# Performance work log

Measured on AMD Instinct MI355X. Metric: run time of the kernel, lower is better.

Reference implementation:

```python
import jax, jax.numpy as jnp
import numpy as np

B, P, K = 32, 1024, 20  # clouds, points per cloud, kNN neighbors
EPS = 1e-5


def knn_idx(x, k):
    # x: [B,P,d] -> indices of k nearest neighbors (squared L2, includes self), [B,P,k]
    d2 = jnp.sum(x * x, axis=-1)
    dist = d2[:, :, None] + d2[:, None, :] - 2.0 * jnp.einsum('bpd,bqd->bpq', x, x)
    _, idx = jax.lax.top_k(-dist, k)
    return idx


def edge_conv(x, idx, msg_fn):
    # gather neighbor features, build [x_i, x_j - x_i] edge features, max-aggregate
    xj = jax.vmap(lambda xb, ib: xb[ib])(x, idx)            # [B,P,K,d]
    xi = jnp.broadcast_to(x[:, :, None, :], xj.shape)       # [B,P,K,d]
    e = jnp.concatenate([xi, xj - xi], axis=-1)             # [B,P,K,2d]
    return jnp.max(msg_fn(e), axis=2)                       # [B,P,out]


def setup_inputs() -> dict:
    key = jax.random.key(0)
    ks = jax.random.split(key, 5)
    s = 0.05
    return {
        'pos': jax.random.normal(ks[0], (B * P, 3), jnp.float32),
        'W1a': jax.random.normal(ks[1], (6, 64), jnp.float32) * s,
        'b1a': jnp.zeros((64,), jnp.float32),
        'g1': jnp.ones((64,), jnp.float32),
        'be1': jnp.zeros((64,), jnp.float32),
        'W1b': jax.random.normal(ks[2], (64, 64), jnp.float32) * s,
        'b1b': jnp.zeros((64,), jnp.float32),
        'W2': jax.random.normal(ks[3], (128, 128), jnp.float32) * s,
        'b2': jnp.zeros((128,), jnp.float32),
        'Wl': jax.random.normal(ks[4], (192, 128), jnp.float32) * s,
        'bl': jnp.zeros((128,), jnp.float32),
        'batch': jnp.repeat(jnp.arange(B, dtype=jnp.int32), P),
    }


def reference(pos, W1a, b1a, g1, be1, W1b, b1b, W2, b2, Wl, bl, batch):
    # batch is uniform-sized and sorted -> fixed reshape to [B,P,.]
    x0 = pos.reshape(B, P, 3)

    def mlp1(e):  # Linear(6,64) -> BatchNorm -> ReLU -> Linear(64,64)
        h = e @ W1a + b1a
        mu = jnp.mean(h, axis=(0, 1, 2))
        var = jnp.var(h, axis=(0, 1, 2))
        h = (h - mu) * jax.lax.rsqrt(var + EPS) * g1 + be1
        h = jax.nn.relu(h)
        return h @ W1b + b1b

    x1 = edge_conv(x0, knn_idx(x0, K), mlp1)                         # [B,P,64]
    x2 = edge_conv(x1, knn_idx(x1, K), lambda e: e @ W2 + b2)        # [B,P,128]
    h = jnp.concatenate([x1, x2], axis=-1) @ Wl + bl                 # [B,P,128]
    return jnp.max(h, axis=1)                                        # global_max_pool -> [B,128]
```

## Files before the change

kernel.cpp:

```cpp
#include <hip/hip_runtime.h>
#include <cfloat>
#include <cstdint>

#define NB 32
#define NP 1024
#define NK 20
#define NPTS 32768

typedef __attribute__((ext_vector_type(8))) short bf16x8;
typedef __attribute__((ext_vector_type(4))) float f32x4;

__device__ __forceinline__ unsigned bf16rne(float v) {
  const unsigned u = __float_as_uint(v);
  return (u + 0x7fffu + ((u >> 16) & 1u)) >> 16;
}

__global__ __launch_bounds__(256) void kd2(const float* __restrict__ x, int dim,
                                           float* __restrict__ d2) {
  int p = blockIdx.x * 256 + threadIdx.x;
  if (p >= NPTS) return;
  if (dim == 64) {
    const float4* xr = (const float4*)(x + (size_t)p * 64);
    float s = 0.f;
#pragma unroll
    for (int dq = 0; dq < 16; dq++) {
      float4 v = xr[dq];
      s = fmaf(v.x, v.x, s);
      s = fmaf(v.y, v.y, s);
      s = fmaf(v.z, v.z, s);
      s = fmaf(v.w, v.w, s);
    }
    d2[p] = s;
  } else {
    float s = 0.f;
#pragma unroll
    for (int d = 0; d < 3; d++) {
      float v = x[p * 3 + d];
      s = fmaf(v, v, s);
    }
    d2[p] = s;
  }
}

__global__ __launch_bounds__(256) void kxprep(const float* __restrict__ x,
                                              unsigned short* __restrict__ Xh,
                                              unsigned short* __restrict__ Xl) {
  const int t = blockIdx.x * 256 + threadIdx.x;
  const int p = t >> 3, g = t & 7;
  const float4* xr = (const float4*)(x + (size_t)p * 64 + g * 8);
  const float4 v0 = xr[0];
  const float4 v1 = xr[1];
  const float vv[8] = {v0.x, v0.y, v0.z, v0.w, v1.x, v1.y, v1.z, v1.w};
  unsigned short h[8], l[8];
#pragma unroll
  for (int j = 0; j < 8; j++) {
    const float z = vv[j];
    const unsigned u = __float_as_uint(z);
    const unsigned hb = (u + 0x7fffu + ((u >> 16) & 1u)) & 0xffff0000u;
    h[j] = (unsigned short)(hb >> 16);
    l[j] = (unsigned short)bf16rne(z - __uint_as_float(hb));
  }
  const int off = (((p >> 4) * 2 + (g >> 2)) * 64 + ((g & 3) << 4) + (p & 15)) * 8;
  *(uint4*)&Xh[off] = *(const uint4*)&h[0];
  *(uint4*)&Xl[off] = *(const uint4*)&l[0];
}

__global__ __launch_bounds__(256) void kdistm(const unsigned short* __restrict__ Xh,
                                              const unsigned short* __restrict__ Xl,
                                              const float* __restrict__ d2,
                                              int c0, int nc, float* __restrict__ D) {
  const int lane = threadIdx.x & 63;
  const int w = threadIdx.x >> 6;
  const int cloud = blockIdx.x % nc;
  const int t = blockIdx.x / nc;
  const int tr0 = (t >> 3) * 128, tc0 = (t & 7) * 128;
  const int cb = (c0 + cloud) * 1024;
  const int rw = tr0 + w * 32;

  bf16x8 Ah[2][2], Al[2][2];
#pragma unroll
  for (int mt = 0; mt < 2; mt++)
#pragma unroll
    for (int ks = 0; ks < 2; ks++) {
      const int tg = (cb + rw + mt * 16) >> 4;
      const size_t base = ((size_t)(tg * 2 + ks) * 64 + lane) * 8;
      Ah[mt][ks] = *(const bf16x8*)&Xh[base];
      Al[mt][ks] = *(const bf16x8*)&Xl[base];
    }
  float d2r[2][4];
#pragma unroll
  for (int mt = 0; mt < 2; mt++)
#pragma unroll
    for (int r = 0; r < 4; r++)
      d2r[mt][r] = d2[cb + rw + mt * 16 + (lane >> 4) * 4 + r];

  for (int nt = 0; nt < 8; nt++) {
    const int cg = cb + tc0 + nt * 16;
    bf16x8 Bh2[2], Bl2[2];
#pragma unroll
    for (int ks = 0; ks < 2; ks++) {
      const int tg = cg >> 4;
      const size_t base = ((size_t)(tg * 2 + ks) * 64 + lane) * 8;
      Bh2[ks] = *(const bf16x8*)&Xh[base];
      Bl2[ks] = *(const bf16x8*)&Xl[base];
    }
    const float d2c = d2[cg + (lane & 15)];
#pragma unroll
    for (int mt = 0; mt < 2; mt++) {
      f32x4 C = {0.f, 0.f, 0.f, 0.f};
      C = __builtin_amdgcn_mfma_f32_16x16x32_bf16(Ah[mt][0], Bh2[0], C, 0, 0, 0);
      C = __builtin_amdgcn_mfma_f32_16x16x32_bf16(Ah[mt][0], Bl2[0], C, 0, 0, 0);
      C = __builtin_amdgcn_mfma_f32_16x16x32_bf16(Al[mt][0], Bh2[0], C, 0, 0, 0);
      C = __builtin_amdgcn_mfma_f32_16x16x32_bf16(Ah[mt][1], Bh2[1], C, 0, 0, 0);
      C = __builtin_amdgcn_mfma_f32_16x16x32_bf16(Ah[mt][1], Bl2[1], C, 0, 0, 0);
      C = __builtin_amdgcn_mfma_f32_16x16x32_bf16(Al[mt][1], Bh2[1], C, 0, 0, 0);
#pragma unroll
      for (int r = 0; r < 4; r++) {
        const int row = cloud * 1024 + rw + mt * 16 + (lane >> 4) * 4 + r;
        const int col = tc0 + nt * 16 + (lane & 15);
        D[(size_t)row * 1024 + col] = fmaf(-2.f, C[r], d2r[mt][r] + d2c);
      }
    }
  }
}

template <int DIM>
__global__ __launch_bounds__(256) void kdist(const float* __restrict__ x,
                                             const float* __restrict__ d2,
                                             int c0, int nc, float* __restrict__ D) {
  constexpr int KC = (DIM == 64) ? 32 : 3;
  __shared__ float As[KC][132];
  __shared__ float Bs[KC][132];
  const int tid = threadIdx.x;
  const int cloud = blockIdx.x % nc;
  const int t = blockIdx.x / nc;
  const int tr0 = (t >> 3) * 128, tc0 = (t & 7) * 128;
  const int cb = (c0 + cloud) * 1024;
  const int tr = tid >> 4, tc = tid & 15;

  float acc[8][8];
#pragma unroll
  for (int i = 0; i < 8; i++)
#pragma unroll
    for (int j = 0; j < 8; j++) acc[i][j] = 0.f;

  for (int kc = 0; kc < DIM; kc += KC) {
    __syncthreads();
    if constexpr (DIM == 64) {
      const int row = tid >> 1, seg = tid & 1;
      const float4* sa = (const float4*)(x + (size_t)(cb + tr0 + row) * 64 + kc + seg * 16);
      const float4* sb = (const float4*)(x + (size_t)(cb + tc0 + row) * 64 + kc + seg * 16);
#pragma unroll
      for (int i = 0; i < 4; i++) {
        float4 va = sa[i];
        float4 vb = sb[i];
        const int k0 = seg * 16 + i * 4;
        As[k0 + 0][row] = va.x;
        As[k0 + 1][row] = va.y;
        As[k0 + 2][row] = va.z;
        As[k0 + 3][row] = va.w;
        Bs[k0 + 0][row] = vb.x;
        Bs[k0 + 1][row] = vb.y;
        Bs[k0 + 2][row] = vb.z;
        Bs[k0 + 3][row] = vb.w;
      }
    } else {
      if (tid < 128) {
#pragma unroll
        for (int d = 0; d < 3; d++) {
          As[d][tid] = x[(size_t)(cb + tr0 + tid) * 3 + d];
          Bs[d][tid] = x[(size_t)(cb + tc0 + tid) * 3 + d];
        }
      }
    }
    __syncthreads();
#pragma unroll
    for (int k = 0; k < KC; k++) {
      float a[8], b[8];
      *(float4*)&a[0] = *(const float4*)&As[k][tr * 8];
      *(float4*)&a[4] = *(const float4*)&As[k][tr * 8 + 4];
      *(float4*)&b[0] = *(const float4*)&Bs[k][tc * 8];
      *(float4*)&b[4] = *(const float4*)&Bs[k][tc * 8 + 4];
#pragma unroll
      for (int i = 0; i < 8; i++)
#pragma unroll
        for (int j = 0; j < 8; j++) acc[i][j] = fmaf(a[i], b[j], acc[i][j]);
    }
  }
  float d2r[8], d2c[8];
#pragma unroll
  for (int i = 0; i < 8; i++) d2r[i] = d2[cb + tr0 + tr * 8 + i];
#pragma unroll
  for (int j = 0; j < 8; j++) d2c[j] = d2[cb + tc0 + tc * 8 + j];
#pragma unroll
  for (int i = 0; i < 8; i++) {
    float o[8];
#pragma unroll
    for (int j = 0; j < 8; j++) o[j] = fmaf(-2.f, acc[i][j], d2r[i] + d2c[j]);
    float* dst = &D[(size_t)(cloud * 1024 + tr0 + tr * 8 + i) * 1024 + tc0 + tc * 8];
    *(float4*)&dst[0] = *(const float4*)&o[0];
    *(float4*)&dst[4] = *(const float4*)&o[4];
  }
}

__global__ __launch_bounds__(256) void kselect(const float* __restrict__ D,
                                               int c0, int* __restrict__ idxo) {
  __shared__ unsigned long long lw[4][64];
  const int lane = threadIdx.x & 63;
  const int sub = threadIdx.x >> 6;
  const int pchunk = blockIdx.x * 4 + sub;
  const int pg = c0 * 1024 + pchunk;
  const int gbase = (pg >> 10) << 10;

  unsigned k32[16];
  const float4* dr = (const float4*)(D + (size_t)pchunk * 1024 + lane * 4);
#pragma unroll
  for (int i = 0; i < 4; i++) {
    const float4 d4 = dr[i * 64];
    const float dv[4] = {d4.x, d4.y, d4.z, d4.w};
#pragma unroll
    for (int j = 0; j < 4; j++) {
      unsigned u = __float_as_uint(dv[j]);
      u ^= (((int)u >> 31) | 0x80000000u);
      k32[i * 4 + j] = u;
    }
  }

  unsigned mn = k32[0], mx = k32[0];
#pragma unroll
  for (int i = 1; i < 16; i++) {
    mn = k32[i] < mn ? k32[i] : mn;
    mx = k32[i] > mx ? k32[i] : mx;
  }
#pragma unroll
  for (int s = 1; s < 64; s <<= 1) {
    const unsigned a = __shfl_xor(mn, s, 64);
    const unsigned b = __shfl_xor(mx, s, 64);
    mn = a < mn ? a : mn;
    mx = b > mx ? b : mx;
  }

  unsigned long long midk = 0;
  bool found = false;
  {
    unsigned long long lo = mn, hi = (unsigned long long)mx + 1;
    for (int it = 0; it < 33 && !found; ++it) {
      if (hi - lo <= 1) break;
      const unsigned long long m2 = lo + ((hi - lo) >> 1);
      const unsigned m32 = (unsigned)m2;
      int cnt = 0;
#pragma unroll
      for (int i = 0; i < 16; i++) cnt += (k32[i] < m32) ? 1 : 0;
#pragma unroll
      for (int s = 1; s < 64; s <<= 1) cnt += __shfl_xor(cnt, s, 64);
      if (cnt < 20)
        lo = m2;
      else if (cnt > 63)
        hi = m2;
      else {
        midk = (m2 << 10);
        found = true;
      }
    }
  }
  if (!found) {
    unsigned long long key[16];
#pragma unroll
    for (int i = 0; i < 4; i++)
#pragma unroll
      for (int j = 0; j < 4; j++)
        key[i * 4 + j] = ((unsigned long long)k32[i * 4 + j] << 10) |
                         (unsigned)(i * 256 + lane * 4 + j);
    unsigned long long mn64 = key[0], mx64 = key[0];
#pragma unroll
    for (int i = 1; i < 16; i++) {
      mn64 = key[i] < mn64 ? key[i] : mn64;
      mx64 = key[i] > mx64 ? key[i] : mx64;
    }
#pragma unroll
    for (int s = 1; s < 64; s <<= 1) {
      const unsigned long long a = __shfl_xor(mn64, s, 64);
      const unsigned long long b = __shfl_xor(mx64, s, 64);
      mn64 = a < mn64 ? a : mn64;
      mx64 = b > mx64 ? b : mx64;
    }
    unsigned long long lo = mn64, hi = mx64 + 1;
    bool f2 = false;
    for (int it = 0; it < 48 && !f2; ++it) {
      const unsigned long long m2 = lo + ((hi - lo) >> 1);
      int cnt = 0;
#pragma unroll
      for (int i = 0; i < 16; i++) cnt += (key[i] < m2) ? 1 : 0;
#pragma unroll
      for (int s = 1; s < 64; s <<= 1) cnt += __shfl_xor(cnt, s, 64);
      if (cnt < 20)
        lo = m2;
      else if (cnt > 63)
        hi = m2;
      else {
        midk = m2;
        f2 = true;
      }
    }
  }

  unsigned mask = 0;
  unsigned long long key64[16];
#pragma unroll
  for (int i = 0; i < 4; i++)
#pragma unroll
    for (int j = 0; j < 4; j++) {
      const int ii = i * 4 + j;
      key64[ii] = ((unsigned long long)k32[ii] << 10) |
                  (unsigned)(i * 256 + lane * 4 + j);
      mask |= (key64[ii] < midk) ? (1u << ii) : 0u;
    }
  const int lc = __popc(mask);
  int x = lc;
#pragma unroll
  for (int s = 1; s < 64; s <<= 1) {
    const int y = __shfl_up(x, s, 64);
    if (lane >= s) x += y;
  }
  int off = x - lc;
  unsigned long long* w = lw[sub];
  w[lane] = ~0ULL;
  __builtin_amdgcn_wave_barrier();
#pragma unroll
  for (int i = 0; i < 16; i++) {
    if ((mask & (1u << i)) && off < 64) {
      w[off] = key64[i];
      off++;
    }
  }
  __builtin_amdgcn_wave_barrier();
  const unsigned long long K = w[lane];
  int rank = 0;
#pragma unroll
  for (int m = 0; m < 64; m++) rank += (K > w[m]) ? 1 : 0;
  if (K != ~0ULL && rank < NK)
    idxo[(size_t)pg * NK + rank] = gbase + (int)(K & 1023u);
}

__global__ __launch_bounds__(256) void kstats(const float* __restrict__ pos,
                                              const int* __restrict__ idx,
                                              double* __restrict__ Spart) {
  __shared__ float red[4][42];
  const int tid = threadIdx.x;
  const int w = tid >> 6;
  int p = blockIdx.x * 256 + tid;
  float xi0 = pos[p * 3], xi1 = pos[p * 3 + 1], xi2 = pos[p * 3 + 2];
  float s1[6];
  float s2[36];
#pragma unroll
  for (int a = 0; a < 6; a++) s1[a] = 0.f;
#pragma unroll
  for (int a = 0; a < 36; a++) s2[a] = 0.f;
  for (int k = 0; k < NK; k++) {
    int j = idx[p * NK + k];
    float e[6];
    e[0] = xi0;
    e[1] = xi1;
    e[2] = xi2;
    e[3] = pos[j * 3] - xi0;
    e[4] = pos[j * 3 + 1] - xi1;
    e[5] = pos[j * 3 + 2] - xi2;
#pragma unroll
    for (int a = 0; a < 6; a++) {
      s1[a] += e[a];
#pragma unroll
      for (int b = 0; b < 6; b++) s2[a * 6 + b] = fmaf(e[a], e[b], s2[a * 6 + b]);
    }
  }
#pragma unroll
  for (int a = 0; a < 6; a++) {
#pragma unroll
    for (int m = 1; m < 64; m <<= 1) s1[a] += __shfl_xor(s1[a], m, 64);
  }
#pragma unroll
  for (int a = 0; a < 36; a++) {
#pragma unroll
    for (int m = 1; m < 64; m <<= 1) s2[a] += __shfl_xor(s2[a], m, 64);
  }
  if ((tid & 63) == 0) {
#pragma unroll
    for (int a = 0; a < 6; a++) red[w][a] = s1[a];
#pragma unroll
    for (int a = 0; a < 36; a++) red[w][6 + a] = s2[a];
  }
  __syncthreads();
  if (tid < 42) {
    double t = (double)red[0][tid] + (double)red[1][tid] + (double)red[2][tid] +
               (double)red[3][tid];
    Spart[(size_t)blockIdx.x * 42 + tid] = t;
  }
}

__global__ void kbn(const double* __restrict__ Spart, const float* __restrict__ W1a,
                    const float* __restrict__ b1a, const float* __restrict__ g1,
                    const float* __restrict__ be1, const float* __restrict__ W1b,
                    float* __restrict__ ss, unsigned short* __restrict__ Bh,
                    unsigned short* __restrict__ Bl) {
  __shared__ double S[42];
  const int c = threadIdx.x;
  if (c < 42) {
    double t = 0.0;
    for (int b = 0; b < 128; b++) t += Spart[(size_t)b * 42 + c];
    S[c] = t;
  }
  for (int t = c; t < 4096; t += 256) {
    const int j = t & 7, L = (t >> 3) & 63, f = t >> 9;
    const int nt = f >> 1, ks = f & 1;
    const int k = ks * 32 + (L >> 4) * 8 + j;
    const int n = nt * 16 + (L & 15);
    const float wv = W1b[k * 64 + n];
    const unsigned u = __float_as_uint(wv);
    const unsigned hb = (u + 0x7fffu + ((u >> 16) & 1u)) & 0xffff0000u;
    Bh[t] = (unsigned short)(hb >> 16);
    Bl[t] = (unsigned short)bf16rne(wv - __uint_as_float(hb));
  }
  __syncthreads();
  if (c < 64) {
    double w[6];
#pragma unroll
    for (int d = 0; d < 6; d++) w[d] = (double)W1a[d * 64 + c];
    double b = (double)b1a[c];
    const double invN = 1.0 / (double)((size_t)NPTS * NK);
    double m1 = 0.0;
#pragma unroll
    for (int d = 0; d < 6; d++) m1 += w[d] * S[d];
    m1 *= invN;
    double q = 0.0;
#pragma unroll
    for (int a = 0; a < 6; a++)
#pragma unroll
      for (int d = 0; d < 6; d++) q += w[a] * w[d] * S[6 + a * 6 + d];
    q *= invN;
    double mu = m1 + b;
    double eh2 = q + 2.0 * b * m1 + b * b;
    double var = eh2 - mu * mu;
    if (var < 0.0) var = 0.0;
    double inv = 1.0 / sqrt(var + 1e-5);
    double sc = (double)g1[c] * inv;
    ss[c] = (float)sc;
    ss[64 + c] = (float)((double)be1[c] - mu * sc);
  }
}

#define EC1P 8
__global__ __launch_bounds__(256) void kec1(const float* __restrict__ pos,
                                            const int* __restrict__ idx,
                                            const float* __restrict__ ss,
                                            const float* __restrict__ W1a,
                                            const float* __restrict__ b1a,
                                            const unsigned short* __restrict__ Bh,
                                            const unsigned short* __restrict__ Bl,
                                            const float* __restrict__ b1b,
                                            float* __restrict__ x1) {
  __shared__ __align__(16) unsigned short Ah[4][3072];
  __shared__ __align__(16) unsigned short Al[4][3072];
  __shared__ float nbr[4][160];
  const int tid = threadIdx.x;
  const int lane = tid & 63;
  const int w = tid >> 6;
  const int p0 = blockIdx.x * EC1P + w * 2;

  unsigned short* ah = Ah[w];
  unsigned short* al = Al[w];
  float* nb = nbr[w];

  if (lane < 40) {
    const int j = idx[(size_t)p0 * NK + lane];
    nb[lane * 4 + 0] = pos[j * 3 + 0];
    nb[lane * 4 + 1] = pos[j * 3 + 1];
    nb[lane * 4 + 2] = pos[j * 3 + 2];
  }

  float wdf[3], wbt[3];
#pragma unroll
  for (int d = 0; d < 3; d++) {
    const float top = W1a[d * 64 + lane];
    const float bot = W1a[(3 + d) * 64 + lane];
    wdf[d] = top - bot;
    wbt[d] = bot;
  }
  const float b1 = b1a[lane];
  const float sc = ss[lane];
  const float sh = ss[64 + lane];
  const int lanepart = ((lane >> 5) * 512) + (((lane & 31) >> 3) * 128) + (lane & 7);
  __builtin_amdgcn_wave_barrier();

#pragma unroll
  for (int pp = 0; pp < 2; pp++) {
    const int p = p0 + pp;
    const float xi0 = pos[p * 3], xi1 = pos[p * 3 + 1], xi2 = pos[p * 3 + 2];
    const float pu = fmaf(xi2, wdf[2], fmaf(xi1, wdf[1], fmaf(xi0, wdf[0], b1)));
    for (int k = 0; k < NK; k++) {
      const int row = pp * NK + k;
      const float4 nbv = *(const float4*)&nb[row * 4];
      const float pv = fmaf(nbv.z, wbt[2], fmaf(nbv.y, wbt[1], nbv.x * wbt[0]));
      const float z = fmaxf(fmaf(pu + pv, sc, sh), 0.f);
      const unsigned u = __float_as_uint(z);
      const unsigned hb = (u + 0x7fffu + ((u >> 16) & 1u)) & 0xffff0000u;
      const int off = (row >> 4) * 1024 + (row & 15) * 8 + lanepart;
      ah[off] = (unsigned short)(hb >> 16);
      al[off] = (unsigned short)bf16rne(z - __uint_as_float(hb));
    }
  }
  __builtin_amdgcn_wave_barrier();

  bf16x8 bh[4][2], bl[4][2];
#pragma unroll
  for (int nt = 0; nt < 4; nt++)
#pragma unroll
    for (int ks = 0; ks < 2; ks++) {
      const int base = ((nt * 2 + ks) * 64 + lane) * 8;
      bh[nt][ks] = *(const bf16x8*)&Bh[base];
      bl[nt][ks] = *(const bf16x8*)&Bl[base];
    }

  float pA[4], pB[4];
#pragma unroll
  for (int nt = 0; nt < 4; nt++) {
    pA[nt] = -FLT_MAX;
    pB[nt] = -FLT_MAX;
  }
  const int q4 = (lane >> 4) * 4;

#pragma unroll
  for (int mt = 0; mt < 3; mt++) {
    const bf16x8 a_h0 = *(const bf16x8*)&ah[mt * 1024 + lane * 8];
    const bf16x8 a_l0 = *(const bf16x8*)&al[mt * 1024 + lane * 8];
    const bf16x8 a_h1 = *(const bf16x8*)&ah[mt * 1024 + 512 + lane * 8];
    const bf16x8 a_l1 = *(const bf16x8*)&al[mt * 1024 + 512 + lane * 8];
#pragma unroll
    for (int nt = 0; nt < 4; nt++) {
      f32x4 C = {0.f, 0.f, 0.f, 0.f};
      C = __builtin_amdgcn_mfma_f32_16x16x32_bf16(a_h0, bh[nt][0], C, 0, 0, 0);
      C = __builtin_amdgcn_mfma_f32_16x16x32_bf16(a_h0, bl[nt][0], C, 0, 0, 0);
      C = __builtin_amdgcn_mfma_f32_16x16x32_bf16(a_l0, bh[nt][0], C, 0, 0, 0);
      C = __builtin_amdgcn_mfma_f32_16x16x32_bf16(a_h1, bh[nt][1], C, 0, 0, 0);
      C = __builtin_amdgcn_mfma_f32_16x16x32_bf16(a_h1, bl[nt][1], C, 0, 0, 0);
      C = __builtin_amdgcn_mfma_f32_16x16x32_bf16(a_l1, bh[nt][1], C, 0, 0, 0);
#pragma unroll
      for (int r = 0; r < 4; r++) {
        const int row = mt * 16 + q4 + r;
        const float vv = C[r];
        if (row < NK) pA[nt] = fmaxf(pA[nt], vv);
        if (row >= NK && row < 2 * NK) pB[nt] = fmaxf(pB[nt], vv);
      }
    }
  }
#pragma unroll
  for (int s = 16; s < 64; s <<= 1) {
#pragma unroll
    for (int nt = 0; nt < 4; nt++) {
      pA[nt] = fmaxf(pA[nt], __shfl_xor(pA[nt], s, 64));
      pB[nt] = fmaxf(pB[nt], __shfl_xor(pB[nt], s, 64));
    }
  }
  if (lane < 16) {
#pragma unroll
    for (int nt = 0; nt < 4; nt++) {
      const float bb = b1b[nt * 16 + lane];
      x1[(size_t)p0 * 64 + nt * 16 + lane] = pA[nt] + bb;
      x1[(size_t)(p0 + 1) * 64 + nt * 16 + lane] = pB[nt] + bb;
    }
  }
}

__global__ __launch_bounds__(256) void kv(const float* __restrict__ x1,
                                          const float* __restrict__ W2,
                                          float* __restrict__ v) {
  const int c = threadIdx.x & 127;
  const int sub = threadIdx.x >> 7;
  float wv[64];
#pragma unroll
  for (int d = 0; d < 64; d++) wv[d] = W2[(64 + d) * 128 + c];
  const int pbase = blockIdx.x * 64 + sub * 32;
  for (int i = 0; i < 32; i++) {
    const int p = pbase + i;
    const float4* xr = (const float4*)(x1 + (size_t)p * 64);
    float a0 = 0.f, a1 = 0.f;
#pragma unroll
    for (int dq = 0; dq < 16; dq++) {
      float4 xv = xr[dq];
      a0 = fmaf(xv.x, wv[dq * 4 + 0], a0);
      a1 = fmaf(xv.y, wv[dq * 4 + 1], a1);
      a0 = fmaf(xv.z, wv[dq * 4 + 2], a0);
      a1 = fmaf(xv.w, wv[dq * 4 + 3], a1);
    }
    v[(size_t)p * 128 + c] = a0 + a1;
  }
}

__global__ __launch_bounds__(256) void kprep(const float* __restrict__ W2,
                                             const float* __restrict__ Wl,
                                             const float* __restrict__ b2,
                                             const float* __restrict__ bl,
                                             float* __restrict__ Bc,
                                             float* __restrict__ cb) {
  const int t = blockIdx.x * 256 + threadIdx.x;
  const int d = t >> 7, c = t & 127;
  float s = Wl[d * 128 + c];
  for (int e = 0; e < 128; e++)
    s = fmaf(W2[d * 128 + e] - W2[(64 + d) * 128 + e], Wl[(64 + e) * 128 + c], s);
  Bc[d * 128 + c] = s;
  Bc[(64 + 2 * d) * 128 + c] = Wl[(64 + 2 * d) * 128 + c];
  Bc[(64 + 2 * d + 1) * 128 + c] = Wl[(64 + 2 * d + 1) * 128 + c];
  if (d == 0) {
    float sb = bl[c];
    for (int e = 0; e < 128; e++) sb = fmaf(b2[e], Wl[(64 + e) * 128 + c], sb);
    cb[c] = sb;
  }
}

#define ATS 72
#define BSS 132
__global__ __launch_bounds__(256) void kgemm(const float* __restrict__ x1,
                                             const float* __restrict__ v,
                                             const int* __restrict__ idx,
                                             const float* __restrict__ Bc,
                                             float* __restrict__ partial) {
  __shared__ float AT[192 * ATS];
  __shared__ float BS[16 * BSS];
  int* idxs = (int*)BS;
  const int tid = threadIdx.x;
  const int cloud = blockIdx.x & 31;
  const int mb = blockIdx.x >> 5;
  const int pbase = cloud * 1024 + mb * 64;

#pragma unroll
  for (int r = 0; r < 5; r++) {
    int id = r * 256 + tid;
    idxs[id] = idx[(size_t)pbase * NK + id];
  }
#pragma unroll
  for (int r = 0; r < 16; r++) {
    int id = r * 256 + tid;
    int m = id >> 6, k = id & 63;
    AT[k * ATS + m] = x1[(size_t)(pbase + m) * 64 + k];
  }
  __syncthreads();
#pragma unroll
  for (int r = 0; r < 32; r++) {
    int id = r * 256 + tid;
    int m = id >> 7, kk = id & 127;
    const int* ip = &idxs[m * NK];
    float mx = -FLT_MAX;
#pragma unroll
    for (int k = 0; k < NK; k++) mx = fmaxf(mx, v[(size_t)ip[k] * 128 + kk]);
    AT[(64 + kk) * ATS + m] = mx;
  }
  __syncthreads();

  const int tr = tid >> 4, tc = tid & 15;
  float acc[4][8];
#pragma unroll
  for (int i = 0; i < 4; i++)
#pragma unroll
    for (int n = 0; n < 8; n++) acc[i][n] = 0.f;
  for (int kc = 0; kc < 12; kc++) {
#pragma unroll
    for (int r = 0; r < 8; r++) {
      int id = r * 256 + tid;
      int row = id >> 7, col = id & 127;
      BS[row * BSS + col] = Bc[(size_t)(kc * 16 + row) * 128 + col];
    }
    __syncthreads();
#pragma unroll
    for (int k = 0; k < 16; k++) {
      int kg = kc * 16 + k;
      float4 a = *(const float4*)&AT[kg * ATS + tr * 4];
      float4 b0 = *(const float4*)&BS[k * BSS + tc * 8];
      float4 b1 = *(const float4*)&BS[k * BSS + tc * 8 + 4];
      float av[4] = {a.x, a.y, a.z, a.w};
      float bv[8] = {b0.x, b0.y, b0.z, b0.w, b1.x, b1.y, b1.z, b1.w};
#pragma unroll
      for (int i = 0; i < 4; i++)
#pragma unroll
        for (int n = 0; n < 8; n++) acc[i][n] = fmaf(av[i], bv[n], acc[i][n]);
    }
    __syncthreads();
  }
#pragma unroll
  for (int n = 0; n < 8; n++) {
    float m4 = fmaxf(fmaxf(acc[0][n], acc[1][n]), fmaxf(acc[2][n], acc[3][n]));
    BS[tr * BSS + tc * 8 + n] = m4;
  }
  __syncthreads();
  if (tid < 128) {
    float m = -FLT_MAX;
#pragma unroll
    for (int rr = 0; rr < 16; rr++) m = fmaxf(m, BS[rr * BSS + tid]);
    partial[(size_t)(cloud * 16 + mb) * 128 + tid] = m;
  }
}

__global__ __launch_bounds__(256) void kred(const float* __restrict__ partial,
                                            const float* __restrict__ cb,
                                            float* __restrict__ out) {
  int t = blockIdx.x * 256 + threadIdx.x;
  int b = t >> 7, c = t & 127;
  float m = -FLT_MAX;
#pragma unroll
  for (int mb = 0; mb < 16; mb++) m = fmaxf(m, partial[(size_t)(b * 16 + mb) * 128 + c]);
  out[t] = m + cb[c];
}

extern "C" void kernel_launch(void* const* d_in, const int* in_sizes, int n_in,
                              void* d_out, int out_size, void* d_ws, size_t ws_size,
                              hipStream_t stream) {
  const float* pos = (const float*)d_in[0];
  const float* W1a = (const float*)d_in[1];
  const float* b1a = (const float*)d_in[2];
  const float* g1 = (const float*)d_in[3];
  const float* be1 = (const float*)d_in[4];
  const float* W1b = (const float*)d_in[5];
  const float* b1b = (const float*)d_in[6];
  const float* W2 = (const float*)d_in[7];
  const float* b2 = (const float*)d_in[8];
  const float* Wl = (const float*)d_in[9];
  const float* bl = (const float*)d_in[10];
  float* out = (float*)d_out;

  float* ws = (float*)d_ws;
  float* x1 = ws;
  float* v = ws + 2097152;
  int* idx = (int*)(ws + 6291456);
  float* d2b = ws + 6946816;
  double* Spart = (double*)(ws + 6979584);
  float* Bc = ws + 6990336;
  float* cb = ws + 7014912;
  float* ss = ws + 7015040;
  unsigned short* Bh = (unsigned short*)(ws + 7015168);
  unsigned short* Bl = (unsigned short*)(ws + 7017216);
  float* partial = ws + 7019264;
  unsigned short* Xfh = (unsigned short*)(ws + 7084800);
  unsigned short* Xfl = (unsigned short*)(ws + 8133376);
  const size_t base = 9181952;
  float* D = ws + base;

  if (ws_size < (base + 1024 * 1024) * sizeof(float)) return;

  size_t avail = ws_size / sizeof(float) - base;
  int nc = 1;
  for (int c = 32; c >= 1; c >>= 1)
    if ((size_t)c * 1024 * 1024 <= avail) {
      nc = c;
      break;
    }

  kd2<<<128, 256, 0, stream>>>(pos, 3, d2b);
  for (int c0 = 0; c0 < NB; c0 += nc) {
    kdist<3><<<nc * 64, 256, 0, stream>>>(pos, d2b, c0, nc, D);
    kselect<<<nc * 256, 256, 0, stream>>>(D, c0, idx);
  }

  kstats<<<128, 256, 0, stream>>>(pos, idx, Spart);
  kbn<<<1, 256, 0, stream>>>(Spart, W1a, b1a, g1, be1, W1b, ss, Bh, Bl);
  kec1<<<NPTS / EC1P, 256, 0, stream>>>(pos, idx, ss, W1a, b1a, Bh, Bl, b1b, x1);

  kd2<<<128, 256, 0, stream>>>(x1, 64, d2b);
  kxprep<<<1024, 256, 0, stream>>>(x1, Xfh, Xfl);
  for (int c0 = 0; c0 < NB; c0 += nc) {
    kdistm<<<nc * 64, 256, 0, stream>>>(Xfh, Xfl, d2b, c0, nc, D);
    kselect<<<nc * 256, 256, 0, stream>>>(D, c0, idx);
  }

  kv<<<512, 256, 0, stream>>>(x1, W2, v);
  kprep<<<32, 256, 0, stream>>>(W2, Wl, b2, bl, Bc, cb);
  kgemm<<<512, 256, 0, stream>>>(x1, v, idx, Bc, partial);
  kred<<<16, 256, 0, stream>>>(partial, cb, out);
}
```

Baseline: 371.6 us.

## Fuse 3D distance computation into top-k selection and use ballot-based counting

```diff
diff --git a/kernel.cpp b/kernel.cpp
--- a/kernel.cpp
+++ b/kernel.cpp
@@ -124,87 +124,196 @@
   }
 }
 
-template <int DIM>
-__global__ __launch_bounds__(256) void kdist(const float* __restrict__ x,
-                                             const float* __restrict__ d2,
-                                             int c0, int nc, float* __restrict__ D) {
-  constexpr int KC = (DIM == 64) ? 32 : 3;
-  __shared__ float As[KC][132];
-  __shared__ float Bs[KC][132];
+__device__ __forceinline__ void select20(const float* dv, unsigned long long* w,
+                                         int lane, int pg, int gbase,
+                                         int* __restrict__ idxo) {
+  unsigned k32[16];
+#pragma unroll
+  for (int ii = 0; ii < 16; ii++) {
+    unsigned u = __float_as_uint(dv[ii]);
+    u ^= (((int)u >> 31) | 0x80000000u);
+    k32[ii] = u;
+  }
+  unsigned lmn = k32[0];
+#pragma unroll
+  for (int ii = 1; ii < 16; ii++) lmn = k32[ii] < lmn ? k32[ii] : lmn;
+  unsigned mn = lmn, mxm = lmn;
+#pragma unroll
+  for (int s = 1; s < 64; s <<= 1) {
+    const unsigned a = __shfl_xor(mn, s, 64);
+    const unsigned b = __shfl_xor(mxm, s, 64);
+    mn = a < mn ? a : mn;
+    mxm = b > mxm ? b : mxm;
+  }
+  unsigned lo = mn;
+  unsigned long long hi = (unsigned long long)mxm + 1;
+  unsigned m32 = 0;
+  bool found = false;
+  for (int it = 0; it < 34; ++it) {
+    if (hi - lo <= 1) break;
+    const unsigned m = (unsigned)(lo + ((hi - (unsigned long long)lo) >> 1));
+    int cnt = 0;
+#pragma unroll
+    for (int ii = 0; ii < 16; ii++) cnt += __popcll(__ballot(k32[ii] < m));
+    if (cnt < 20)
+      lo = m;
+    else if (cnt > 63)
+      hi = m;
+    else {
+      m32 = m;
+      found = true;
+      break;
+    }
+  }
+
+  if (found) {
+    unsigned mask = 0;
+    unsigned long long key64[16];
+#pragma unroll
+    for (int i = 0; i < 4; i++)
+#pragma unroll
+      for (int j = 0; j < 4; j++) {
+        const int ii = i * 4 + j;
+        key64[ii] = ((unsigned long long)k32[ii] << 10) |
+                    (unsigned)(i * 256 + (lane << 2) + j);
+        mask |= (k32[ii] < m32) ? (1u << ii) : 0u;
+      }
+    const int lc = __popc(mask);
+    int x = lc;
+#pragma unroll
+    for (int s = 1; s < 64; s <<= 1) {
+      const int y = __shfl_up(x, s, 64);
+      if (lane >= s) x += y;
+    }
+    int off = x - lc;
+    w[lane] = ~0ULL;
+    __builtin_amdgcn_wave_barrier();
+#pragma unroll
+    for (int ii = 0; ii < 16; ii++) {
+      if (mask & (1u << ii)) {
+        w[off] = key64[ii];
+        off++;
+      }
+    }
+    __builtin_amdgcn_wave_barrier();
+    const unsigned long long K = w[lane];
+    unsigned long long lo64 = ((unsigned long long)lo) << 10;
+    unsigned long long hi64 = ((unsigned long long)m32) << 10;
+    unsigned long long cut = hi64;
+    for (int it = 0; it < 48 && (hi64 - lo64) > 1; ++it) {
+      const unsigned long long m = lo64 + ((hi64 - lo64) >> 1);
+      const int cnt = __popcll(__ballot(K < m));
+      if (cnt == 20) {
+        cut = m;
+        break;
+      }
+      if (cnt < 20)
+        lo64 = m;
+      else
+        hi64 = m;
+      cut = hi64;
+    }
+    const unsigned long long sel = __ballot(K < cut);
+    if (K < cut) {
+      const int slot = __builtin_amdgcn_mbcnt_hi(
+          (unsigned)(sel >> 32), __builtin_amdgcn_mbcnt_lo((unsigned)sel, 0));
+      idxo[(size_t)pg * NK + slot] = gbase + (int)(K & 1023u);
+    }
+  } else {
+    unsigned long long key64[16];
+#pragma unroll
+    for (int i = 0; i < 4; i++)
+#pragma unroll
+      for (int j = 0; j < 4; j++) {
+        const int ii = i * 4 + j;
+        key64[ii] = ((unsigned long long)k32[ii] << 10) |
+                    (unsigned)(i * 256 + (lane << 2) + j);
+      }
+    unsigned long long lo64 = ((unsigned long long)lo) << 10;
+    unsigned long long hi64 = hi << 10;
+    unsigned long long cut = hi64;
+    for (int it = 0; it < 48 && (hi64 - lo64) > 1; ++it) {
+      const unsigned long long m = lo64 + ((hi64 - lo64) >> 1);
+      int cnt = 0;
+#pragma unroll
+      for (int ii = 0; ii < 16; ii++) cnt += __popcll(__ballot(key64[ii] < m));
+      if (cnt == 20) {
+        cut = m;
+        break;
+      }
+      if (cnt < 20)
+        lo64 = m;
+      else
+        hi64 = m;
+      cut = hi64;
+    }
+    int base = 0;
+#pragma unroll
+    for (int ii = 0; ii < 16; ii++) {
+      const unsigned long long b = __ballot(key64[ii] < cut);
+      if (key64[ii] < cut) {
+        const int slot = base + __builtin_amdgcn_mbcnt_hi(
+                                    (unsigned)(b >> 32),
+                                    __builtin_amdgcn_mbcnt_lo((unsigned)b, 0));
+        idxo[(size_t)pg * NK + slot] = gbase + (int)(key64[ii] & 1023u);
+      }
+      base += __popcll(b);
+    }
+  }
+}
+
+__global__ __launch_bounds__(256) void kfsel1(const float* __restrict__ pos,
+                                              const float* __restrict__ d2,
+                                              int* __restrict__ idxo) {
+  __shared__ float px[1024], py[1024], pz[1024], pd2[1024];
+  __shared__ unsigned long long lw[4][64];
   const int tid = threadIdx.x;
-  const int cloud = blockIdx.x % nc;
-  const int t = blockIdx.x / nc;
-  const int tr0 = (t >> 3) * 128, tc0 = (t & 7) * 128;
-  const int cb = (c0 + cloud) * 1024;
-  const int tr = tid >> 4, tc = tid & 15;
-
-  float acc[8][8];
-#pragma unroll
-  for (int i = 0; i < 8; i++)
-#pragma unroll
-    for (int j = 0; j < 8; j++) acc[i][j] = 0.f;
-
-  for (int kc = 0; kc < DIM; kc += KC) {
-    __syncthreads();
-    if constexpr (DIM == 64) {
-      const int row = tid >> 1, seg = tid & 1;
-      const float4* sa = (const float4*)(x + (size_t)(cb + tr0 + row) * 64 + kc + seg * 16);
-      const float4* sb = (const float4*)(x + (size_t)(cb + tc0 + row) * 64 + kc + seg * 16);
-#pragma unroll
-      for (int i = 0; i < 4; i++) {
-        float4 va = sa[i];
-        float4 vb = sb[i];
-        const int k0 = seg * 16 + i * 4;
-        As[k0 + 0][row] = va.x;
-        As[k0 + 1][row] = va.y;
-        As[k0 + 2][row] = va.z;
-        As[k0 + 3][row] = va.w;
-        Bs[k0 + 0][row] = vb.x;
-        Bs[k0 + 1][row] = vb.y;
-        Bs[k0 + 2][row] = vb.z;
-        Bs[k0 + 3][row] = vb.w;
-      }
-    } else {
-      if (tid < 128) {
-#pragma unroll
-        for (int d = 0; d < 3; d++) {
-          As[d][tid] = x[(size_t)(cb + tr0 + tid) * 3 + d];
-          Bs[d][tid] = x[(size_t)(cb + tc0 + tid) * 3 + d];
-        }
-      }
-    }
-    __syncthreads();
-#pragma unroll
-    for (int k = 0; k < KC; k++) {
-      float a[8], b[8];
-      *(float4*)&a[0] = *(const float4*)&As[k][tr * 8];
-      *(float4*)&a[4] = *(const float4*)&As[k][tr * 8 + 4];
-      *(float4*)&b[0] = *(const float4*)&Bs[k][tc * 8];
-      *(float4*)&b[4] = *(const float4*)&Bs[k][tc * 8 + 4];
-#pragma unroll
-      for (int i = 0; i < 8; i++)
-#pragma unroll
-        for (int j = 0; j < 8; j++) acc[i][j] = fmaf(a[i], b[j], acc[i][j]);
-    }
-  }
-  float d2r[8], d2c[8];
-#pragma unroll
-  for (int i = 0; i < 8; i++) d2r[i] = d2[cb + tr0 + tr * 8 + i];
-#pragma unroll
-  for (int j = 0; j < 8; j++) d2c[j] = d2[cb + tc0 + tc * 8 + j];
-#pragma unroll
-  for (int i = 0; i < 8; i++) {
-    float o[8];
-#pragma unroll
-    for (int j = 0; j < 8; j++) o[j] = fmaf(-2.f, acc[i][j], d2r[i] + d2c[j]);
-    float* dst = &D[(size_t)(cloud * 1024 + tr0 + tr * 8 + i) * 1024 + tc0 + tc * 8];
-    *(float4*)&dst[0] = *(const float4*)&o[0];
-    *(float4*)&dst[4] = *(const float4*)&o[4];
-  }
-}
-
-__global__ __launch_bounds__(256) void kselect(const float* __restrict__ D,
-                                               int c0, int* __restrict__ idxo) {
+  const int lane = tid & 63;
+  const int w = tid >> 6;
+  const int cloud = blockIdx.x >> 6;
+  const int mb = blockIdx.x & 63;
+  const int cb = cloud << 10;
+
+  {
+    const float4* ppos = (const float4*)(pos + (size_t)cb * 3 + tid * 12);
+    const float4 a = ppos[0], b = ppos[1], c = ppos[2];
+    *(float4*)&px[tid * 4] = make_float4(a.x, a.w, b.z, c.y);
+    *(float4*)&py[tid * 4] = make_float4(a.y, b.x, b.w, c.z);
+    *(float4*)&pz[tid * 4] = make_float4(a.z, b.y, c.x, c.w);
+    *(float4*)&pd2[tid * 4] = *(const float4*)(d2 + cb + tid * 4);
+  }
+  __syncthreads();
+
+  for (int pp = 0; pp < 4; pp++) {
+    const int pl = mb * 16 + w * 4 + pp;
+    const float xi0 = px[pl], xi1 = py[pl], xi2 = pz[pl];
+    const float dp = pd2[pl];
+    float dv[16];
+#pragma unroll
+    for (int i = 0; i < 4; i++) {
+      const float4 X = *(const float4*)&px[i * 256 + lane * 4];
+      const float4 Y = *(const float4*)&py[i * 256 + lane * 4];
+      const float4 Z = *(const float4*)&pz[i * 256 + lane * 4];
+      const float4 Q = *(const float4*)&pd2[i * 256 + lane * 4];
+      const float xs[4] = {X.x, X.y, X.z, X.w};
+      const float ys[4] = {Y.x, Y.y, Y.z, Y.w};
+      const float zs[4] = {Z.x, Z.y, Z.z, Z.w};
+      const float qs[4] = {Q.x, Q.y, Q.z, Q.w};
+#pragma unroll
+      for (int j = 0; j < 4; j++) {
+        float acc = 0.f;
+        acc = fmaf(xi0, xs[j], acc);
+        acc = fmaf(xi1, ys[j], acc);
+        acc = fmaf(xi2, zs[j], acc);
+        dv[i * 4 + j] = fmaf(-2.f, acc, dp + qs[j]);
+      }
+    }
+    select20(dv, lw[w], lane, cb + pl, cb, idxo);
+  }
+}
+
+__global__ __launch_bounds__(256) void kselect2(const float* __restrict__ D,
+                                                int c0, int* __restrict__ idxo) {
   __shared__ unsigned long long lw[4][64];
   const int lane = threadIdx.x & 63;
   const int sub = threadIdx.x >> 6;
@@ -212,134 +321,17 @@
   const int pg = c0 * 1024 + pchunk;
   const int gbase = (pg >> 10) << 10;
 
-  unsigned k32[16];
+  float dv[16];
   const float4* dr = (const float4*)(D + (size_t)pchunk * 1024 + lane * 4);
 #pragma unroll
   for (int i = 0; i < 4; i++) {
     const float4 d4 = dr[i * 64];
-    const float dv[4] = {d4.x, d4.y, d4.z, d4.w};
-#pragma unroll
-    for (int j = 0; j < 4; j++) {
-      unsigned u = __float_as_uint(dv[j]);
-      u ^= (((int)u >> 31) | 0x80000000u);
-      k32[i * 4 + j] = u;
-    }
-  }
-
-  unsigned mn = k32[0], mx = k32[0];
-#pragma unroll
-  for (int i = 1; i < 16; i++) {
-    mn = k32[i] < mn ? k32[i] : mn;
-    mx = k32[i] > mx ? k32[i] : mx;
-  }
-#pragma unroll
-  for (int s = 1; s < 64; s <<= 1) {
-    const unsigned a = __shfl_xor(mn, s, 64);
-    const unsigned b = __shfl_xor(mx, s, 64);
-    mn = a < mn ? a : mn;
-    mx = b > mx ? b : mx;
-  }
-
-  unsigned long long midk = 0;
-  bool found = false;
-  {
-    unsigned long long lo = mn, hi = (unsigned long long)mx + 1;
-    for (int it = 0; it < 33 && !found; ++it) {
-      if (hi - lo <= 1) break;
-      const unsigned long long m2 = lo + ((hi - lo) >> 1);
-      const unsigned m32 = (unsigned)m2;
-      int cnt = 0;
-#pragma unroll
-      for (int i = 0; i < 16; i++) cnt += (k32[i] < m32) ? 1 : 0;
-#pragma unroll
-      for (int s = 1; s < 64; s <<= 1) cnt += __shfl_xor(cnt, s, 64);
-      if (cnt < 20)
-        lo = m2;
-      else if (cnt > 63)
-        hi = m2;
-      else {
-        midk = (m2 << 10);
-        found = true;
-      }
-    }
-  }
-  if (!found) {
-    unsigned long long key[16];
-#pragma unroll
-    for (int i = 0; i < 4; i++)
-#pragma unroll
-      for (int j = 0; j < 4; j++)
-        key[i * 4 + j] = ((unsigned long long)k32[i * 4 + j] << 10) |
-                         (unsigned)(i * 256 + lane * 4 + j);
-    unsigned long long mn64 = key[0], mx64 = key[0];
-#pragma unroll
-    for (int i = 1; i < 16; i++) {
-      mn64 = key[i] < mn64 ? key[i] : mn64;
-      mx64 = key[i] > mx64 ? key[i] : mx64;
-    }
-#pragma unroll
-    for (int s = 1; s < 64; s <<= 1) {
-      const unsigned long long a = __shfl_xor(mn64, s, 64);
-      const unsigned long long b = __shfl_xor(mx64, s, 64);
-      mn64 = a < mn64 ? a : mn64;
-      mx64 = b > mx64 ? b : mx64;
-    }
-    unsigned long long lo = mn64, hi = mx64 + 1;
-    bool f2 = false;
-    for (int it = 0; it < 48 && !f2; ++it) {
-      const unsigned long long m2 = lo + ((hi - lo) >> 1);
-      int cnt = 0;
-#pragma unroll
-      for (int i = 0; i < 16; i++) cnt += (key[i] < m2) ? 1 : 0;
-#pragma unroll
-      for (int s = 1; s < 64; s <<= 1) cnt += __shfl_xor(cnt, s, 64);
-      if (cnt < 20)
-        lo = m2;
-      else if (cnt > 63)
-        hi = m2;
-      else {
-        midk = m2;
-        f2 = true;
-      }
-    }
-  }
-
-  unsigned mask = 0;
-  unsigned long long key64[16];
-#pragma unroll
-  for (int i = 0; i < 4; i++)
-#pragma unroll
-    for (int j = 0; j < 4; j++) {
-      const int ii = i * 4 + j;
-      key64[ii] = ((unsigned long long)k32[ii] << 10) |
-                  (unsigned)(i * 256 + lane * 4 + j);
-      mask |= (key64[ii] < midk) ? (1u << ii) : 0u;
-    }
-  const int lc = __popc(mask);
-  int x = lc;
-#pragma unroll
-  for (int s = 1; s < 64; s <<= 1) {
-    const int y = __shfl_up(x, s, 64);
-    if (lane >= s) x += y;
-  }
-  int off = x - lc;
-  unsigned long long* w = lw[sub];
-  w[lane] = ~0ULL;
-  __builtin_amdgcn_wave_barrier();
-#pragma unroll
-  for (int i = 0; i < 16; i++) {
-    if ((mask & (1u << i)) && off < 64) {
-      w[off] = key64[i];
-      off++;
-    }
-  }
-  __builtin_amdgcn_wave_barrier();
-  const unsigned long long K = w[lane];
-  int rank = 0;
-#pragma unroll
-  for (int m = 0; m < 64; m++) rank += (K > w[m]) ? 1 : 0;
-  if (K != ~0ULL && rank < NK)
-    idxo[(size_t)pg * NK + rank] = gbase + (int)(K & 1023u);
+    dv[i * 4 + 0] = d4.x;
+    dv[i * 4 + 1] = d4.y;
+    dv[i * 4 + 2] = d4.z;
+    dv[i * 4 + 3] = d4.w;
+  }
+  select20(dv, lw[sub], lane, pg, gbase, idxo);
 }
 
 __global__ __launch_bounds__(256) void kstats(const float* __restrict__ pos,
@@ -752,10 +744,7 @@
     }
 
   kd2<<<128, 256, 0, stream>>>(pos, 3, d2b);
-  for (int c0 = 0; c0 < NB; c0 += nc) {
-    kdist<3><<<nc * 64, 256, 0, stream>>>(pos, d2b, c0, nc, D);
-    kselect<<<nc * 256, 256, 0, stream>>>(D, c0, idx);
-  }
+  kfsel1<<<NB * 64, 256, 0, stream>>>(pos, d2b, idx);
 
   kstats<<<128, 256, 0, stream>>>(pos, idx, Spart);
   kbn<<<1, 256, 0, stream>>>(Spart, W1a, b1a, g1, be1, W1b, ss, Bh, Bl);
@@ -765,7 +754,7 @@
   kxprep<<<1024, 256, 0, stream>>>(x1, Xfh, Xfl);
   for (int c0 = 0; c0 < NB; c0 += nc) {
     kdistm<<<nc * 64, 256, 0, stream>>>(Xfh, Xfl, d2b, c0, nc, D);
-    kselect<<<nc * 256, 256, 0, stream>>>(D, c0, idx);
+    kselect2<<<nc * 256, 256, 0, stream>>>(D, c0, idx);
   }
 
   kv<<<512, 256, 0, stream>>>(x1, W2, v);
```

Result: faster. 352.8 us (-5.1%).
